# Optimization experiments

Hardware: AMD Instinct MI355X
Metric: run time of the kernel (lower is better)

## Reference

```python
import jax, jax.numpy as jnp
import numpy as np

PATCH_SIZE = 3
T = 1.0


def _aggregate_one(v, shift_map, cost_map):
    # v: (C, H, W); shift_map: (2, K, H, W) int; cost_map: (K, H, W)
    p = PATCH_SIZE // 2
    K, H, W = cost_map.shape
    # pad cost with high value (10 -> near-zero softmax weight), shifts with 10 (junk, clamped later)
    pc = jnp.pad(cost_map, ((0, 0), (p, p), (p, p)), constant_values=10.0)
    ps = jnp.pad(shift_map, ((0, 0), (0, 0), (p, p), (p, p)), constant_values=10)
    costs, sis, sjs = [], [], []
    for di in range(PATCH_SIZE):          # small fixed loop (patch_size^2 = 9)
        for dj in range(PATCH_SIZE):
            costs.append(pc[:, di:di + H, dj:dj + W])
            sis.append(ps[0, :, di:di + H, dj:dj + W] + (p - di))
            sjs.append(ps[1, :, di:di + H, dj:dj + W] + (p - dj))
    all_cost = jnp.concatenate(costs, axis=0)                # (P2K, H, W)
    ii = jnp.clip(jnp.concatenate(sis, axis=0), 0, v.shape[1] - 1)
    jj = jnp.clip(jnp.concatenate(sjs, axis=0), 0, v.shape[2] - 1)
    w = jax.nn.softmax(-all_cost / T, axis=0)                # softmax over P2K candidates
    gathered = v[:, ii, jj]                                  # (C, P2K, H, W) irregular gather
    return jnp.sum(w[None] * gathered, axis=1)               # (C, H, W)


def setup_inputs() -> dict:
    key = jax.random.key(0)
    k1, k2, k3 = jax.random.split(key, 3)
    B, C, H, W, K = 2, 32, 256, 256, 4
    v = jax.random.normal(k1, (B, C, H, W), dtype=jnp.float32)
    cost_map = jax.random.uniform(k2, (B, K, H, W), dtype=jnp.float32)
    shift_map = jax.random.randint(k3, (B, 2, K, H, W), 0, H).astype(jnp.int64)
    return {"v": v, "cost_map": cost_map, "shift_map": shift_map}


def reference(v, cost_map, shift_map):
    # Batched PSAttentionMasked.forward with aggregation=True;
    # shift_map/cost_map stand in for the opaque PatchMatch custom kernel output.
    return jax.vmap(_aggregate_one)(v, shift_map, cost_map)
```

## Files before the change

kernel.cpp:

```cpp
#include <hip/hip_runtime.h>
#include <hip/hip_fp16.h>

#define B_ 2
#define C_ 32
#define H_ 256
#define W_ 256
#define K_ 4
#define HW_ (H_ * W_)

__global__ __launch_bounds__(256) void transpose_v_kernel(
    const float* __restrict__ v, unsigned int* __restrict__ vt) {
  __shared__ float tile[32][65];
  int t = threadIdx.x;
  int pix0 = blockIdx.x * 64;
  int b = pix0 >> 16;
  int pixb = pix0 & (HW_ - 1);
  const float* vb = v + (size_t)b * C_ * HW_;
#pragma unroll
  for (int it = 0; it < 8; ++it) {
    int c = (t >> 6) + it * 4;
    int px = t & 63;
    tile[c][px] = __builtin_nontemporal_load(&vb[(size_t)c * HW_ + pixb + px]);
  }
  __syncthreads();
  unsigned int* vtb = vt + (size_t)pix0 * (C_ / 2);
#pragma unroll
  for (int it = 0; it < 4; ++it) {
    int px = (t >> 4) + it * 16;
    int c2 = t & 15;
    float lo = tile[2 * c2][px];
    float hi = tile[2 * c2 + 1][px];
    __half2 h = __floats2half2_rn(lo, hi);
    unsigned int bits;
    __builtin_memcpy(&bits, &h, 4);
    __builtin_nontemporal_store(bits, &vtb[px * 16 + c2]);
  }
}

__global__ __launch_bounds__(128, 3) void psatt_kernel(
    const float* __restrict__ cost_map, const int* __restrict__ shift_map,
    const unsigned int* __restrict__ vt, float* __restrict__ out) {
  __shared__ float2 lds_eo[36][32];
  __shared__ float lds_part[32][4];
  __shared__ float lds_out[32][33];

  int t = threadIdx.x;
  int bid = blockIdx.x;
  int xcd = bid & 7;
  int slot = bid >> 3;
  int b = xcd >> 2;
  int workid = ((xcd & 3) << 9) + slot;
  int y = workid >> 3;
  int x0 = (workid & 7) << 5;

  {
    int k = t >> 5;
    int px = t & 31;
    int x = x0 + px;
    const float* cm = cost_map + (size_t)(b * K_ + k) * HW_;
    const int* s0 = shift_map + (size_t)((b * 2 + 0) * K_ + k) * HW_;
    const int* s1 = shift_map + (size_t)((b * 2 + 1) * K_ + k) * HW_;
    float psum = 0.f;
#pragma unroll
    for (int di = 0; di < 3; ++di) {
      int ny = y + di - 1;
      bool yin = (unsigned)ny < (unsigned)H_;
#pragma unroll
      for (int dj = 0; dj < 3; ++dj) {
        int nx = x + dj - 1;
        bool inb = yin && ((unsigned)nx < (unsigned)W_);
        int nidx = ny * W_ + nx;
        float cost;
        int si, sj;
        if (inb) {
          cost = cm[nidx];
          si = s0[nidx] + (1 - di);
          sj = s1[nidx] + (1 - dj);
        } else {
          cost = 10.0f;
          si = 11 - di;
          sj = 11 - dj;
        }
        float e = __expf(-cost);
        int ii = min(max(si, 0), H_ - 1);
        int jj = min(max(sj, 0), W_ - 1);
        int m = k * 9 + di * 3 + dj;
        lds_eo[m][px] = make_float2(e, __int_as_float((ii * W_ + jj) << 6));
        psum += e;
      }
    }
    lds_part[px][k] = psum;
  }
  __syncthreads();

  {
    int q = t & 3;
    int px = t >> 2;
    const char* base = (const char*)vt + (size_t)b * HW_ * 64;
    unsigned int qoff = (unsigned int)(q << 4);
    float acc[8] = {0.f, 0.f, 0.f, 0.f, 0.f, 0.f, 0.f, 0.f};
#pragma unroll
    for (int half = 0; half < 2; ++half) {
      uint4 hv[18];
      float ew[18];
#pragma unroll
      for (int m = 0; m < 18; ++m) {
        float2 eo = lds_eo[half * 18 + m][px];
        ew[m] = eo.x;
        unsigned int voff = (unsigned int)__float_as_int(eo.y) + qoff;
        hv[m] = *(const uint4*)(base + voff);
      }
#pragma unroll
      for (int m = 0; m < 18; ++m) {
        float e = ew[m];
        __half2 h0, h1, h2, h3;
        __builtin_memcpy(&h0, &hv[m].x, 4);
        __builtin_memcpy(&h1, &hv[m].y, 4);
        __builtin_memcpy(&h2, &hv[m].z, 4);
        __builtin_memcpy(&h3, &hv[m].w, 4);
        float2 f0 = __half22float2(h0);
        float2 f1 = __half22float2(h1);
        float2 f2 = __half22float2(h2);
        float2 f3 = __half22float2(h3);
        acc[0] += e * f0.x; acc[1] += e * f0.y;
        acc[2] += e * f1.x; acc[3] += e * f1.y;
        acc[4] += e * f2.x; acc[5] += e * f2.y;
        acc[6] += e * f3.x; acc[7] += e * f3.y;
      }
    }
    float4 ps = *(const float4*)&lds_part[px][0];
    float inv = 1.0f / (ps.x + ps.y + ps.z + ps.w);
#pragma unroll
    for (int j = 0; j < 8; ++j) {
      lds_out[px][8 * q + j] = acc[j] * inv;
    }
  }
  __syncthreads();

  {
    int px = t & 31;
#pragma unroll
    for (int it = 0; it < 8; ++it) {
      int c = (t >> 5) + it * 4;
      __builtin_nontemporal_store(
          lds_out[px][c],
          &out[((size_t)(b * C_ + c) * H_ + y) * W_ + x0 + px]);
    }
  }
}

extern "C" void kernel_launch(void* const* d_in, const int* in_sizes, int n_in,
                              void* d_out, int out_size, void* d_ws, size_t ws_size,
                              hipStream_t stream) {
  const float* v = (const float*)d_in[0];
  const float* cost_map = (const float*)d_in[1];
  const int* shift_map = (const int*)d_in[2];
  float* out = (float*)d_out;

  unsigned int* vt = (unsigned int*)d_ws;
  const int grid = B_ * H_ * (W_ / 32);

  transpose_v_kernel<<<B_ * HW_ / 64, 256, 0, stream>>>(v, vt);
  psatt_kernel<<<grid, 128, 0, stream>>>(cost_map, shift_map, vt, out);
}
```

Baseline: 44.92 us.

## Vectorize transpose loads/stores and shrink attention blocks to 16-pixel single-wave tiles

The transpose kernel now reads v with 16-byte vector loads and writes each pixel's 64-byte fp16 record as one 16-byte store per thread, replacing scalar accesses. The attention kernel is retiled from 32-pixel, 128-thread blocks to 16-pixel, 64-thread blocks with a doubled grid and higher occupancy hint. The shared weight/offset table is transposed to a padded [px][m] layout. These changes aim to cut memory instruction count and raise the number of resident waves for latency hiding, at the cost of more blocks, more per-block overhead, and shorter 64-byte output store runs per channel row.

New measurement: 44.46 us. Within noise of the previous version (-1.0%).

```diff
diff --git a/kernel.cpp b/kernel.cpp
--- a/kernel.cpp
+++ b/kernel.cpp
@@ -8,6 +8,9 @@
 #define K_ 4
 #define HW_ (H_ * W_)
 
+typedef float floatx4 __attribute__((ext_vector_type(4)));
+typedef unsigned int uintx4 __attribute__((ext_vector_type(4)));
+
 __global__ __launch_bounds__(256) void transpose_v_kernel(
     const float* __restrict__ v, unsigned int* __restrict__ vt) {
   __shared__ float tile[32][65];
@@ -16,46 +19,50 @@
   int b = pix0 >> 16;
   int pixb = pix0 & (HW_ - 1);
   const float* vb = v + (size_t)b * C_ * HW_;
+  int c = t >> 3;
+  int f = t & 7;
 #pragma unroll
-  for (int it = 0; it < 8; ++it) {
-    int c = (t >> 6) + it * 4;
-    int px = t & 63;
-    tile[c][px] = __builtin_nontemporal_load(&vb[(size_t)c * HW_ + pixb + px]);
+  for (int h = 0; h < 2; ++h) {
+    int px = h * 32 + f * 4;
+    floatx4 r = __builtin_nontemporal_load(
+        (const floatx4*)&vb[(size_t)c * HW_ + pixb + px]);
+    tile[c][px + 0] = r.x;
+    tile[c][px + 1] = r.y;
+    tile[c][px + 2] = r.z;
+    tile[c][px + 3] = r.w;
   }
   __syncthreads();
-  unsigned int* vtb = vt + (size_t)pix0 * (C_ / 2);
-#pragma unroll
-  for (int it = 0; it < 4; ++it) {
-    int px = (t >> 4) + it * 16;
-    int c2 = t & 15;
-    float lo = tile[2 * c2][px];
-    float hi = tile[2 * c2 + 1][px];
-    __half2 h = __floats2half2_rn(lo, hi);
-    unsigned int bits;
-    __builtin_memcpy(&bits, &h, 4);
-    __builtin_nontemporal_store(bits, &vtb[px * 16 + c2]);
-  }
+  int px = t >> 2, q = t & 3;
+  unsigned int w0, w1, w2, w3;
+  { __half2 h2 = __floats2half2_rn(tile[8*q+0][px], tile[8*q+1][px]); __builtin_memcpy(&w0, &h2, 4); }
+  { __half2 h2 = __floats2half2_rn(tile[8*q+2][px], tile[8*q+3][px]); __builtin_memcpy(&w1, &h2, 4); }
+  { __half2 h2 = __floats2half2_rn(tile[8*q+4][px], tile[8*q+5][px]); __builtin_memcpy(&w2, &h2, 4); }
+  { __half2 h2 = __floats2half2_rn(tile[8*q+6][px], tile[8*q+7][px]); __builtin_memcpy(&w3, &h2, 4); }
+  uintx4 o;
+  o.x = w0; o.y = w1; o.z = w2; o.w = w3;
+  __builtin_nontemporal_store(
+      o, (uintx4*)((char*)vt + ((size_t)(pix0 + px) << 6) + (q << 4)));
 }
 
-__global__ __launch_bounds__(128, 3) void psatt_kernel(
+__global__ __launch_bounds__(64, 6) void psatt_kernel(
     const float* __restrict__ cost_map, const int* __restrict__ shift_map,
     const unsigned int* __restrict__ vt, float* __restrict__ out) {
-  __shared__ float2 lds_eo[36][32];
-  __shared__ float lds_part[32][4];
-  __shared__ float lds_out[32][33];
+  __shared__ float2 lds_ew[16][37];
+  __shared__ float lds_part[16][4];
+  __shared__ float lds_out[16][33];
 
   int t = threadIdx.x;
   int bid = blockIdx.x;
   int xcd = bid & 7;
   int slot = bid >> 3;
   int b = xcd >> 2;
-  int workid = ((xcd & 3) << 9) + slot;
-  int y = workid >> 3;
-  int x0 = (workid & 7) << 5;
+  int workid = ((xcd & 3) << 10) + slot;
+  int y = workid >> 4;
+  int x0 = (workid & 15) << 4;
 
   {
-    int k = t >> 5;
-    int px = t & 31;
+    int k = t >> 4;
+    int px = t & 15;
     int x = x0 + px;
     const float* cm = cost_map + (size_t)(b * K_ + k) * HW_;
     const int* s0 = shift_map + (size_t)((b * 2 + 0) * K_ + k) * HW_;
@@ -85,7 +92,7 @@
         int ii = min(max(si, 0), H_ - 1);
         int jj = min(max(sj, 0), W_ - 1);
         int m = k * 9 + di * 3 + dj;
-        lds_eo[m][px] = make_float2(e, __int_as_float((ii * W_ + jj) << 6));
+        lds_ew[px][m] = make_float2(e, __int_as_float((ii * W_ + jj) << 6));
         psum += e;
       }
     }
@@ -96,7 +103,7 @@
   {
     int q = t & 3;
     int px = t >> 2;
-    const char* base = (const char*)vt + (size_t)b * HW_ * 64;
+    const char* base = (const char*)vt + ((size_t)b * HW_ << 6);
     unsigned int qoff = (unsigned int)(q << 4);
     float acc[8] = {0.f, 0.f, 0.f, 0.f, 0.f, 0.f, 0.f, 0.f};
 #pragma unroll
@@ -105,7 +112,7 @@
       float ew[18];
 #pragma unroll
       for (int m = 0; m < 18; ++m) {
-        float2 eo = lds_eo[half * 18 + m][px];
+        float2 eo = lds_ew[px][half * 18 + m];
         ew[m] = eo.x;
         unsigned int voff = (unsigned int)__float_as_int(eo.y) + qoff;
         hv[m] = *(const uint4*)(base + voff);
@@ -138,10 +145,10 @@
   __syncthreads();
 
   {
-    int px = t & 31;
+    int px = t & 15;
 #pragma unroll
     for (int it = 0; it < 8; ++it) {
-      int c = (t >> 5) + it * 4;
+      int c = (t >> 4) + it * 4;
       __builtin_nontemporal_store(
           lds_out[px][c],
           &out[((size_t)(b * C_ + c) * H_ + y) * W_ + x0 + px]);
@@ -158,8 +165,8 @@
   float* out = (float*)d_out;
 
   unsigned int* vt = (unsigned int*)d_ws;
-  const int grid = B_ * H_ * (W_ / 32);
+  const int grid = B_ * H_ * (W_ / 16);
 
   transpose_v_kernel<<<B_ * HW_ / 64, 256, 0, stream>>>(v, vt);
-  psatt_kernel<<<grid, 128, 0, stream>>>(cost_map, shift_map, vt, out);
+  psatt_kernel<<<grid, 64, 0, stream>>>(cost_map, shift_map, vt, out);
 }
```
